# Performance work log

Measured on AMD Instinct MI355X. Metric: run time of the kernel, lower is better.

## Reference

```python
import jax, jax.numpy as jnp
import numpy as np

NUM_HEADS = 4
LEAKY_SLOPE = 0.2


def setup_inputs() -> dict:
    key = jax.random.key(0)
    k1, k2, k3, k4 = jax.random.split(key, 4)
    B, N, IN_DIM, OUT_DIM = 4, 2048, 256, 256
    head_dim = OUT_DIM // NUM_HEADS
    x = jax.random.normal(k1, (B, N, IN_DIM), dtype=jnp.float32)
    adj = jax.random.randint(k2, (B, N, N), 0, 2).astype(jnp.float32)
    # parameters: W is nn.Linear(in_dim, out_dim, bias=False) -> weight [out, in]
    W = jax.random.normal(k3, (OUT_DIM, IN_DIM), dtype=jnp.float32) * 0.05
    # a is nn.Linear(2*head_dim, 1, bias=False) -> weight [1, 2*head_dim]
    a_w = jax.random.normal(k4, (1, 2 * head_dim), dtype=jnp.float32) * 0.05
    return {"x": x, "adj": adj, "W": W, "a_w": a_w}


def reference(x, adj, W, a_w):
    # Faithful to torch GATLayer.forward in eval mode (dropout = identity).
    B, N, _ = x.shape
    h = jnp.einsum('bnf,of->bno', x, W)                    # [B,N,out_dim]
    h = h.reshape(B, N, NUM_HEADS, -1)                     # [B,N,H,D]
    D = h.shape[-1]
    # Decompose a([h_i, h_j]) = a_src . h_i + a_dst . h_j (same math, no
    # [B,N,N,H,2D] concat materialization).
    a_src, a_dst = a_w[0, :D], a_w[0, D:]
    s_src = jnp.einsum('bnhd,d->bnh', h, a_src)            # [B,N,H]
    s_dst = jnp.einsum('bnhd,d->bnh', h, a_dst)            # [B,N,H]
    e = s_src[:, :, None, :] + s_dst[:, None, :, :]        # [B,N,N,H]
    e = jnp.where(e > 0, e, LEAKY_SLOPE * e)               # LeakyReLU
    # A = ((adj>0) + I) > 0, applied per head
    A = (adj > 0) | jnp.eye(N, dtype=bool)[None]           # [B,N,N]
    e = jnp.where(A[..., None], e, jnp.float32(-1e9))
    alpha = jax.nn.softmax(e, axis=2)                      # softmax over j
    # NOTE: reproduces the original einsum exactly ('bnjh,bnhd->bnhd'):
    # out[b,n,h,d] = (sum_j alpha[b,n,j,h]) * h[b,n,h,d]
    out = jnp.einsum('bnjh,bnhd->bnhd', alpha, h)          # [B,N,H,D]
    return out.reshape(B, N, -1)                           # [B,N,out_dim]
```

## Files before the change

kernel.cpp:

```cpp
#include <hip/hip_runtime.h>


typedef __attribute__((ext_vector_type(8))) short short8;
typedef __attribute__((ext_vector_type(4))) float floatx4;
typedef __attribute__((ext_vector_type(4))) int intx4;

__device__ inline int cvtpk_bf16(float a, float b) {
    int r;
    asm("v_cvt_pk_bf16_f32 %0, %1, %2" : "=v"(r) : "v"(a), "v"(b));
    return r;
}
__device__ inline float lo_bf2f(int p) { return __uint_as_float((unsigned)p << 16); }
__device__ inline float hi_bf2f(int p) { return __uint_as_float((unsigned)p & 0xffff0000u); }

#define LSTR 264

__global__ __launch_bounds__(256) void gat_gemm(const float* __restrict__ X,
                                                const float* __restrict__ W,
                                                float* __restrict__ out) {
    __shared__ short xh[16 * LSTR];
    __shared__ short xl[16 * LSTR];

    const int r0 = blockIdx.x * 16;
    const int t  = threadIdx.x;

    const float4* X4 = (const float4*)(X + (size_t)r0 * 256);
    #pragma unroll
    for (int k = 0; k < 4; ++k) {
        int idx = t + 256 * k;
        int row = idx >> 6;
        int c4  = idx & 63;
        float4 v = X4[idx];
        int h0 = cvtpk_bf16(v.x, v.y);
        int h1 = cvtpk_bf16(v.z, v.w);
        int l0 = cvtpk_bf16(v.x - lo_bf2f(h0), v.y - hi_bf2f(h0));
        int l1 = cvtpk_bf16(v.z - lo_bf2f(h1), v.w - hi_bf2f(h1));
        *(int2*)&xh[row * LSTR + c4 * 4] = make_int2(h0, h1);
        *(int2*)&xl[row * LSTR + c4 * 4] = make_int2(l0, l1);
    }
    __syncthreads();

    const int lane = t & 63;
    const int wave = t >> 6;
    const int q    = lane >> 4;
    const int m    = lane & 15;
    const int o0   = wave * 64;

    floatx4 acc[4] = {};

    #pragma unroll
    for (int it = 0; it < 8; ++it) {
        const int f0 = it * 32 + q * 8;
        short8 ah = *(const short8*)&xh[m * LSTR + f0];
        short8 al = *(const short8*)&xl[m * LSTR + f0];
        #pragma unroll
        for (int nt = 0; nt < 4; ++nt) {
            const float* wp = W + (size_t)(o0 + nt * 16 + m) * 256 + f0;
            float4 w0 = *(const float4*)wp;
            float4 w1 = *(const float4*)(wp + 4);
            int bh0 = cvtpk_bf16(w0.x, w0.y);
            int bh1 = cvtpk_bf16(w0.z, w0.w);
            int bh2 = cvtpk_bf16(w1.x, w1.y);
            int bh3 = cvtpk_bf16(w1.z, w1.w);
            int bl0 = cvtpk_bf16(w0.x - lo_bf2f(bh0), w0.y - hi_bf2f(bh0));
            int bl1 = cvtpk_bf16(w0.z - lo_bf2f(bh1), w0.w - hi_bf2f(bh1));
            int bl2 = cvtpk_bf16(w1.x - lo_bf2f(bh2), w1.y - hi_bf2f(bh2));
            int bl3 = cvtpk_bf16(w1.z - lo_bf2f(bh3), w1.w - hi_bf2f(bh3));
            short8 bh = __builtin_bit_cast(short8, (intx4){bh0, bh1, bh2, bh3});
            short8 bl = __builtin_bit_cast(short8, (intx4){bl0, bl1, bl2, bl3});
            acc[nt] = __builtin_amdgcn_mfma_f32_16x16x32_bf16(ah, bh, acc[nt], 0, 0, 0);
            acc[nt] = __builtin_amdgcn_mfma_f32_16x16x32_bf16(ah, bl, acc[nt], 0, 0, 0);
            acc[nt] = __builtin_amdgcn_mfma_f32_16x16x32_bf16(al, bh, acc[nt], 0, 0, 0);
        }
    }

    #pragma unroll
    for (int nt = 0; nt < 4; ++nt) {
        #pragma unroll
        for (int reg = 0; reg < 4; ++reg) {
            int row = r0 + q * 4 + reg;
            int col = o0 + nt * 16 + m;
            out[(size_t)row * 256 + col] = acc[nt][reg];
        }
    }
}

extern "C" void kernel_launch(void* const* d_in, const int* in_sizes, int n_in,
                              void* d_out, int out_size, void* d_ws, size_t ws_size,
                              hipStream_t stream) {
    const float* x = (const float*)d_in[0];
    const float* W = (const float*)d_in[2];
    float* out     = (float*)d_out;

    gat_gemm<<<512, 256, 0, stream>>>(x, W, out);
}
```

Before: 112.9 us.

## Pre-split W into bf16 hi/lo in a prologue kernel and halve per-block column tile

Adds a small kernel that converts W once into bf16 high and low parts stored in workspace, so the GEMM blocks load ready-made bf16 fragments instead of re-reading fp32 W and re-converting it in every block. The grid is doubled so each block computes 128 output columns instead of 256, which raises parallelism but makes each block restage its 16-row X tile, and X is then converted twice. MFMA operands are swapped so the output is written as float4 rows instead of scalar stores. An extra kernel launch is added.

```diff
diff --git a/kernel.cpp b/kernel.cpp
--- a/kernel.cpp
+++ b/kernel.cpp
@@ -3,7 +3,6 @@
 
 typedef __attribute__((ext_vector_type(8))) short short8;
 typedef __attribute__((ext_vector_type(4))) float floatx4;
-typedef __attribute__((ext_vector_type(4))) int intx4;
 
 __device__ inline int cvtpk_bf16(float a, float b) {
     int r;
@@ -13,15 +12,31 @@
 __device__ inline float lo_bf2f(int p) { return __uint_as_float((unsigned)p << 16); }
 __device__ inline float hi_bf2f(int p) { return __uint_as_float((unsigned)p & 0xffff0000u); }
 
+__global__ __launch_bounds__(256) void split_w(const float* __restrict__ W,
+                                               short* __restrict__ Wh,
+                                               short* __restrict__ Wl) {
+    int gid = blockIdx.x * 256 + threadIdx.x;
+    float4 v = ((const float4*)W)[gid];
+    int h0 = cvtpk_bf16(v.x, v.y);
+    int h1 = cvtpk_bf16(v.z, v.w);
+    int l0 = cvtpk_bf16(v.x - lo_bf2f(h0), v.y - hi_bf2f(h0));
+    int l1 = cvtpk_bf16(v.z - lo_bf2f(h1), v.w - hi_bf2f(h1));
+    *(int2*)(Wh + (size_t)gid * 4) = make_int2(h0, h1);
+    *(int2*)(Wl + (size_t)gid * 4) = make_int2(l0, l1);
+}
+
 #define LSTR 264
 
 __global__ __launch_bounds__(256) void gat_gemm(const float* __restrict__ X,
-                                                const float* __restrict__ W,
+                                                const short* __restrict__ Wh,
+                                                const short* __restrict__ Wl,
                                                 float* __restrict__ out) {
     __shared__ short xh[16 * LSTR];
     __shared__ short xl[16 * LSTR];
 
-    const int r0 = blockIdx.x * 16;
+    const int rb = blockIdx.x >> 1;
+    const int cb = blockIdx.x & 1;
+    const int r0 = rb * 16;
     const int t  = threadIdx.x;
 
     const float4* X4 = (const float4*)(X + (size_t)r0 * 256);
@@ -44,44 +59,30 @@
     const int wave = t >> 6;
     const int q    = lane >> 4;
     const int m    = lane & 15;
-    const int o0   = wave * 64;
+    const int o0   = cb * 128 + wave * 32;
 
-    floatx4 acc[4] = {};
+    floatx4 acc[2] = {};
 
     #pragma unroll
     for (int it = 0; it < 8; ++it) {
         const int f0 = it * 32 + q * 8;
-        short8 ah = *(const short8*)&xh[m * LSTR + f0];
-        short8 al = *(const short8*)&xl[m * LSTR + f0];
+        short8 bxh = *(const short8*)&xh[m * LSTR + f0];
+        short8 bxl = *(const short8*)&xl[m * LSTR + f0];
         #pragma unroll
-        for (int nt = 0; nt < 4; ++nt) {
-            const float* wp = W + (size_t)(o0 + nt * 16 + m) * 256 + f0;
-            float4 w0 = *(const float4*)wp;
-            float4 w1 = *(const float4*)(wp + 4);
-            int bh0 = cvtpk_bf16(w0.x, w0.y);
-            int bh1 = cvtpk_bf16(w0.z, w0.w);
-            int bh2 = cvtpk_bf16(w1.x, w1.y);
-            int bh3 = cvtpk_bf16(w1.z, w1.w);
-            int bl0 = cvtpk_bf16(w0.x - lo_bf2f(bh0), w0.y - hi_bf2f(bh0));
-            int bl1 = cvtpk_bf16(w0.z - lo_bf2f(bh1), w0.w - hi_bf2f(bh1));
-            int bl2 = cvtpk_bf16(w1.x - lo_bf2f(bh2), w1.y - hi_bf2f(bh2));
-            int bl3 = cvtpk_bf16(w1.z - lo_bf2f(bh3), w1.w - hi_bf2f(bh3));
-            short8 bh = __builtin_bit_cast(short8, (intx4){bh0, bh1, bh2, bh3});
-            short8 bl = __builtin_bit_cast(short8, (intx4){bl0, bl1, bl2, bl3});
-            acc[nt] = __builtin_amdgcn_mfma_f32_16x16x32_bf16(ah, bh, acc[nt], 0, 0, 0);
-            acc[nt] = __builtin_amdgcn_mfma_f32_16x16x32_bf16(ah, bl, acc[nt], 0, 0, 0);
-            acc[nt] = __builtin_amdgcn_mfma_f32_16x16x32_bf16(al, bh, acc[nt], 0, 0, 0);
+        for (int nt = 0; nt < 2; ++nt) {
+            const size_t wo = (size_t)(o0 + nt * 16 + m) * 256 + f0;
+            short8 wh8 = *(const short8*)(Wh + wo);
+            short8 wl8 = *(const short8*)(Wl + wo);
+            acc[nt] = __builtin_amdgcn_mfma_f32_16x16x32_bf16(wh8, bxh, acc[nt], 0, 0, 0);
+            acc[nt] = __builtin_amdgcn_mfma_f32_16x16x32_bf16(wl8, bxh, acc[nt], 0, 0, 0);
+            acc[nt] = __builtin_amdgcn_mfma_f32_16x16x32_bf16(wh8, bxl, acc[nt], 0, 0, 0);
         }
     }
 
     #pragma unroll
-    for (int nt = 0; nt < 4; ++nt) {
-        #pragma unroll
-        for (int reg = 0; reg < 4; ++reg) {
-            int row = r0 + q * 4 + reg;
-            int col = o0 + nt * 16 + m;
-            out[(size_t)row * 256 + col] = acc[nt][reg];
-        }
+    for (int nt = 0; nt < 2; ++nt) {
+        float4 v = make_float4(acc[nt][0], acc[nt][1], acc[nt][2], acc[nt][3]);
+        *(float4*)(out + (size_t)(r0 + m) * 256 + o0 + nt * 16 + q * 4) = v;
     }
 }
 
@@ -92,5 +93,9 @@
     const float* W = (const float*)d_in[2];
     float* out     = (float*)d_out;
 
-    gat_gemm<<<512, 256, 0, stream>>>(x, W, out);
+    short* Wh = (short*)d_ws;
+    short* Wl = Wh + 65536;
+
+    split_w<<<64, 256, 0, stream>>>(W, Wh, Wl);
+    gat_gemm<<<1024, 256, 0, stream>>>(x, Wh, Wl, out);
 }
```

Result: slower. 115.8 us (+2.6%).

## Retile GEMM to 32x128 blocks, reuse W fragments, vectorize output stores

Applied to the files above, without the earlier changes.

Each block now covers 32 rows and 128 output columns instead of 16 rows and 256 columns, keeping the grid at 512 blocks. Each converted W fragment (bf16 hi/lo split) now feeds MFMAs for two row tiles, so the per-MFMA cost of W global loads and conversion is halved. The MFMA operands are swapped so each lane holds four consecutive columns, which allows float4 stores in place of scalar stores. In exchange, each X row tile is loaded and split twice (once per column half), and the block uses twice the LDS.

```diff
diff --git a/kernel.cpp b/kernel.cpp
--- a/kernel.cpp
+++ b/kernel.cpp
@@ -18,15 +18,17 @@
 __global__ __launch_bounds__(256) void gat_gemm(const float* __restrict__ X,
                                                 const float* __restrict__ W,
                                                 float* __restrict__ out) {
-    __shared__ short xh[16 * LSTR];
-    __shared__ short xl[16 * LSTR];
+    __shared__ short xh[32 * LSTR];
+    __shared__ short xl[32 * LSTR];
 
-    const int r0 = blockIdx.x * 16;
+    const int rb = blockIdx.x >> 1;
+    const int cb = blockIdx.x & 1;
+    const int r0 = rb * 32;
     const int t  = threadIdx.x;
 
     const float4* X4 = (const float4*)(X + (size_t)r0 * 256);
     #pragma unroll
-    for (int k = 0; k < 4; ++k) {
+    for (int k = 0; k < 8; ++k) {
         int idx = t + 256 * k;
         int row = idx >> 6;
         int c4  = idx & 63;
@@ -44,17 +46,19 @@
     const int wave = t >> 6;
     const int q    = lane >> 4;
     const int m    = lane & 15;
-    const int o0   = wave * 64;
+    const int o0   = cb * 128 + wave * 32;
 
-    floatx4 acc[4] = {};
+    floatx4 acc[2][2] = {};
 
     #pragma unroll
     for (int it = 0; it < 8; ++it) {
         const int f0 = it * 32 + q * 8;
-        short8 ah = *(const short8*)&xh[m * LSTR + f0];
-        short8 al = *(const short8*)&xl[m * LSTR + f0];
+        short8 bxh0 = *(const short8*)&xh[m * LSTR + f0];
+        short8 bxl0 = *(const short8*)&xl[m * LSTR + f0];
+        short8 bxh1 = *(const short8*)&xh[(16 + m) * LSTR + f0];
+        short8 bxl1 = *(const short8*)&xl[(16 + m) * LSTR + f0];
         #pragma unroll
-        for (int nt = 0; nt < 4; ++nt) {
+        for (int nt = 0; nt < 2; ++nt) {
             const float* wp = W + (size_t)(o0 + nt * 16 + m) * 256 + f0;
             float4 w0 = *(const float4*)wp;
             float4 w1 = *(const float4*)(wp + 4);
@@ -66,21 +70,24 @@
             int bl1 = cvtpk_bf16(w0.z - lo_bf2f(bh1), w0.w - hi_bf2f(bh1));
             int bl2 = cvtpk_bf16(w1.x - lo_bf2f(bh2), w1.y - hi_bf2f(bh2));
             int bl3 = cvtpk_bf16(w1.z - lo_bf2f(bh3), w1.w - hi_bf2f(bh3));
-            short8 bh = __builtin_bit_cast(short8, (intx4){bh0, bh1, bh2, bh3});
-            short8 bl = __builtin_bit_cast(short8, (intx4){bl0, bl1, bl2, bl3});
-            acc[nt] = __builtin_amdgcn_mfma_f32_16x16x32_bf16(ah, bh, acc[nt], 0, 0, 0);
-            acc[nt] = __builtin_amdgcn_mfma_f32_16x16x32_bf16(ah, bl, acc[nt], 0, 0, 0);
-            acc[nt] = __builtin_amdgcn_mfma_f32_16x16x32_bf16(al, bh, acc[nt], 0, 0, 0);
+            short8 wh8 = __builtin_bit_cast(short8, (intx4){bh0, bh1, bh2, bh3});
+            short8 wl8 = __builtin_bit_cast(short8, (intx4){bl0, bl1, bl2, bl3});
+            acc[0][nt] = __builtin_amdgcn_mfma_f32_16x16x32_bf16(wh8, bxh0, acc[0][nt], 0, 0, 0);
+            acc[0][nt] = __builtin_amdgcn_mfma_f32_16x16x32_bf16(wl8, bxh0, acc[0][nt], 0, 0, 0);
+            acc[0][nt] = __builtin_amdgcn_mfma_f32_16x16x32_bf16(wh8, bxl0, acc[0][nt], 0, 0, 0);
+            acc[1][nt] = __builtin_amdgcn_mfma_f32_16x16x32_bf16(wh8, bxh1, acc[1][nt], 0, 0, 0);
+            acc[1][nt] = __builtin_amdgcn_mfma_f32_16x16x32_bf16(wl8, bxh1, acc[1][nt], 0, 0, 0);
+            acc[1][nt] = __builtin_amdgcn_mfma_f32_16x16x32_bf16(wh8, bxl1, acc[1][nt], 0, 0, 0);
         }
     }
 
     #pragma unroll
-    for (int nt = 0; nt < 4; ++nt) {
+    for (int rt = 0; rt < 2; ++rt) {
         #pragma unroll
-        for (int reg = 0; reg < 4; ++reg) {
-            int row = r0 + q * 4 + reg;
-            int col = o0 + nt * 16 + m;
-            out[(size_t)row * 256 + col] = acc[nt][reg];
+        for (int nt = 0; nt < 2; ++nt) {
+            float4 v = make_float4(acc[rt][nt][0], acc[rt][nt][1],
+                                   acc[rt][nt][2], acc[rt][nt][3]);
+            *(float4*)(out + (size_t)(r0 + rt * 16 + m) * 256 + o0 + nt * 16 + q * 4) = v;
         }
     }
 }
```

Result: faster. 106.3 us (-5.9%).
